# Kernel tuning notes

Measured on AMD Instinct MI355X. Metric: run time of the kernel, lower is better.

Reference implementation:

```python
import jax, jax.numpy as jnp
import numpy as np

N = 8192  # number of proposals


def setup_inputs() -> dict:
    key = jax.random.key(0)
    k1, k2, k3 = jax.random.split(key, 3)
    xy = jax.random.uniform(k1, (N, 2), dtype=jnp.float32) * 1000.0   # top-left corners
    wh = jax.random.uniform(k2, (N, 2), dtype=jnp.float32) * 120.0 + 4.0  # widths/heights
    conf = jax.random.uniform(k3, (N, 1), dtype=jnp.float32)
    preds = jnp.concatenate([xy, xy + wh, conf], axis=1)  # [N,5] x1,y1,x2,y2,conf
    return {"preds": preds, "thresh": 0.5, "max_proposals": 1000}


def _nms_keep_mask(boxes_sorted, thresh):
    # boxes_sorted: [N,4] sorted by descending confidence
    x1, y1, x2, y2 = (boxes_sorted[:, i] for i in range(4))
    area = (x2 - x1) * (y2 - y1)                               # [N]
    ix1 = jnp.maximum(x1[:, None], x1[None, :])
    iy1 = jnp.maximum(y1[:, None], y1[None, :])
    ix2 = jnp.minimum(x2[:, None], x2[None, :])
    iy2 = jnp.minimum(y2[:, None], y2[None, :])
    iw = jnp.maximum(ix2 - ix1, 0.0)
    ih = jnp.maximum(iy2 - iy1, 0.0)
    inter = iw * ih                                            # [N,N]
    iou = inter / (area[:, None] + area[None, :] - inter + 1e-12)
    n = boxes_sorted.shape[0]
    later = jnp.arange(n)[None, :] > jnp.arange(n)[:, None]    # strictly lower-priority boxes

    def body(i, keep):
        # if box i survives, suppress all later boxes overlapping it above thresh
        sup = keep[i] & later[i] & (iou[i] > thresh)
        return keep & ~sup

    return jax.lax.fori_loop(0, n, body, jnp.ones((n,), dtype=bool))


def reference(preds, thresh, max_proposals):
    # thresh < 0 -> identity (original early return); implemented with thresh >= 0 path
    order = jnp.argsort(-preds[:, 4])          # descending confidence
    boxes_sorted = preds[order, :4]
    keep = _nms_keep_mask(boxes_sorted, thresh)  # [N] bool, in sorted order
    n = preds.shape[0]
    # stable pack: kept positions first (ascending = descending confidence), pad at end
    rank = jnp.where(keep, jnp.arange(n), n)
    pos = jnp.argsort(rank)[:max_proposals]     # [M] positions in sorted order
    valid = keep[pos]                           # [M] which slots are real
    keep_idx = jnp.where(valid, order[pos], -1)  # indices into original preds, -1 pad
    kept = preds[jnp.clip(keep_idx, 0)]          # [M,5]
    kept = jnp.where(valid[:, None], kept, 0.0)
    return kept, keep_idx
```

## Files before the change

kernel.cpp:

```cpp
#include <hip/hip_runtime.h>

typedef unsigned long long u64;

#define FSLOTS 16
#define RCUT 2048

__device__ __forceinline__ u64 bcast64(u64 v, int b) {
  unsigned lo = __builtin_amdgcn_readlane((unsigned)v, b);
  unsigned hi = __builtin_amdgcn_readlane((unsigned)(v >> 32), b);
  return ((u64)hi << 32) | lo;
}
__device__ __forceinline__ u64 sgpr64(u64 v) {
  unsigned lo = __builtin_amdgcn_readfirstlane((unsigned)v);
  unsigned hi = __builtin_amdgcn_readfirstlane((unsigned)(v >> 32));
  return ((u64)hi << 32) | lo;
}
__device__ __forceinline__ u64 wor64(u64 v) {
#pragma unroll
  for (int off = 32; off; off >>= 1) v |= __shfl_xor(v, off, 64);
  return v;
}

#define APPLYJ(JV, T)                                                      \
  if ((T) < lim_) {                                                        \
    int j_ = (JV);                                                         \
    atomicAnd(&live[j_ >> 6], ~((u64)1 << (j_ & 63)));                     \
  }

#define CHUNK(c, BND, RC, LA, LB, LC, LD)                                  \
  if (out < maxp && (c) < nch) {                                           \
    u64 rem_ = sgpr64(live[(c)]);                                          \
    if (rem_) {                                                            \
      u64 K_;                                                              \
      u64 my_ = ((rem_ >> lane) & 1) ? (BND) : 0;                          \
      u64 A_ = sgpr64(wor64(my_));                                         \
      u64 hot_ = rem_ & A_;                                                \
      if (!hot_) {                                                         \
        K_ = rem_;                                                         \
      } else {                                                             \
        u64 defK_ = rem_ & ~A_;                                            \
        u64 myk_ = ((defK_ >> lane) & 1) ? (BND) : 0;                      \
        u64 S_ = sgpr64(wor64(myk_));                                      \
        K_ = defK_;                                                        \
        while (hot_) {                                                     \
          int b_ = __builtin_amdgcn_readfirstlane(                         \
              (int)__builtin_ctzll(hot_));                                 \
          hot_ &= hot_ - 1;                                                \
          if (!((S_ >> b_) & 1)) {                                         \
            K_ |= (u64)1 << b_;                                            \
            S_ |= bcast64(BND, b_);                                        \
          }                                                                \
        }                                                                  \
      }                                                                    \
      int kc_ = (int)__popcll(K_);                                         \
      bool mine_ = (K_ >> lane) & 1;                                       \
      if (mine_) {                                                         \
        int pos_ = out + (int)__popcll(K_ & (((u64)1 << lane) - 1));       \
        if (pos_ < maxp) sel[pos_] = (c) * 64 + lane;                      \
      }                                                                    \
      out += kc_;                                                          \
      if (kc_ > 0 && out < maxp) {                                         \
        int lim_ = mine_ ? ((RC) < FSLOTS ? (RC) : FSLOTS) : 0;            \
        APPLYJ((LA).x, 0)  APPLYJ((LA).y, 1)                               \
        APPLYJ((LA).z, 2)  APPLYJ((LA).w, 3)                               \
        APPLYJ((LB).x, 4)  APPLYJ((LB).y, 5)                               \
        APPLYJ((LB).z, 6)  APPLYJ((LB).w, 7)                               \
        APPLYJ((LC).x, 8)  APPLYJ((LC).y, 9)                               \
        APPLYJ((LC).z, 10) APPLYJ((LC).w, 11)                              \
        APPLYJ((LD).x, 12) APPLYJ((LD).y, 13)                              \
        APPLYJ((LD).z, 14) APPLYJ((LD).w, 15)                              \
        u64 ovf_ = __ballot(mine_ && (RC) > FSLOTS);                       \
        while (ovf_) {                                                     \
          int l_ = (int)__builtin_ctzll(ovf_);                             \
          ovf_ &= ovf_ - 1;                                                \
          int r_ = (c) * 64 + l_;                                          \
          u64 v0_ = (2 * lane < nch)                                       \
                        ? M[(size_t)r_ * nw + 2 * lane] : 0ULL;            \
          u64 v1_ = (2 * lane + 1 < nch)                                   \
                        ? M[(size_t)r_ * nw + 2 * lane + 1] : 0ULL;        \
          live[2 * lane] &= ~v0_;                                          \
          live[2 * lane + 1] &= ~v1_;                                      \
        }                                                                  \
      }                                                                    \
    }                                                                      \
    {                                                                      \
      int cc_ = (c) + 4;                                                   \
      if (cc_ < nch) {                                                     \
        int r_ = cc_ * 64 + lane;                                          \
        int rr_ = r_ < n ? r_ : n - 1;                                     \
        BND = D1[rr_];                                                     \
        RC = rowcnt[rr_];                                                  \
        const int4* lp_ = (const int4*)(rowlist + (size_t)rr_ * FSLOTS);   \
        LA = lp_[0]; LB = lp_[1]; LC = lp_[2]; LD = lp_[3];                \
      }                                                                    \
    }                                                                      \
  }

#define PREF(cc, BND, RC, LA, LB, LC, LD)                                  \
  if ((cc) < nch) {                                                        \
    int r_ = (cc) * 64 + lane;                                             \
    int rr_ = r_ < n ? r_ : n - 1;                                         \
    BND = D1[rr_];                                                         \
    RC = rowcnt[rr_];                                                      \
    const int4* lp_ = (const int4*)(rowlist + (size_t)rr_ * FSLOTS);       \
    LA = lp_[0]; LB = lp_[1]; LC = lp_[2]; LD = lp_[3];                    \
  }

#define SCAN_BODY(NCH_)                                                    \
  int nch = (NCH_);                                                        \
  for (int w = lane; w < 128; w += 64) {                                   \
    u64 m = 0;                                                             \
    if (w < nw) {                                                          \
      long long hi = (long long)(w + 1) * 64;                              \
      m = (hi <= n) ? ~0ULL                                                \
                    : ((n > (long long)w * 64)                             \
                           ? (((u64)1 << (n - w * 64)) - 1) : 0ULL);       \
    }                                                                      \
    live[w] = m;                                                           \
  }                                                                        \
  u64 b0 = 0, b1 = 0, b2 = 0, b3 = 0;                                      \
  int rc0 = 0, rc1 = 0, rc2 = 0, rc3 = 0;                                  \
  int4 l00 = {0,0,0,0}, l01 = {0,0,0,0}, l02 = {0,0,0,0}, l03 = {0,0,0,0}; \
  int4 l10 = {0,0,0,0}, l11 = {0,0,0,0}, l12 = {0,0,0,0}, l13 = {0,0,0,0}; \
  int4 l20 = {0,0,0,0}, l21 = {0,0,0,0}, l22 = {0,0,0,0}, l23 = {0,0,0,0}; \
  int4 l30 = {0,0,0,0}, l31 = {0,0,0,0}, l32 = {0,0,0,0}, l33 = {0,0,0,0}; \
  PREF(0, b0, rc0, l00, l01, l02, l03)                                     \
  PREF(1, b1, rc1, l10, l11, l12, l13)                                     \
  PREF(2, b2, rc2, l20, l21, l22, l23)                                     \
  PREF(3, b3, rc3, l30, l31, l32, l33)                                     \
  int out = 0;                                                             \
  for (int kk = 0; kk < nch && out < maxp; kk += 4) {                      \
    CHUNK(kk + 0, b0, rc0, l00, l01, l02, l03)                             \
    CHUNK(kk + 1, b1, rc1, l10, l11, l12, l13)                             \
    CHUNK(kk + 2, b2, rc2, l20, l21, l22, l23)                             \
    CHUNK(kk + 3, b3, rc3, l30, l31, l32, l33)                             \
  }

__device__ __forceinline__ void do_tile(int wx, int ry, int lane,
                                        const float4* sb4, float4* cb,
                                        float* cbar, int n, float th,
                                        u64* M, u64* D1, int* rowcnt,
                                        int* rowlist, int nw) {
  int col0 = wx * 64;
  int cj = col0 + lane;
  int cjc = cj < n ? cj : n - 1;
  {
    float4 b4 = sb4[cjc];
    cb[lane] = b4;
    cbar[lane] = __fmul_rn(__fsub_rn(b4.z, b4.x), __fsub_rn(b4.w, b4.y));
  }
  int row = ry * 64 + lane;
  if (row >= n) return;
  float4 r4 = sb4[row];
  float rarea = __fmul_rn(__fsub_rn(r4.z, r4.x), __fsub_rn(r4.w, r4.y));
  u64 w = 0;
#pragma unroll 8
  for (int j = 0; j < 64; ++j) {
    float4 c4 = cb[j];
    float ix1 = fmaxf(r4.x, c4.x);
    float iy1 = fmaxf(r4.y, c4.y);
    float ix2 = fminf(r4.z, c4.z);
    float iy2 = fminf(r4.w, c4.w);
    float iw = fmaxf(__fsub_rn(ix2, ix1), 0.0f);
    float ih = fmaxf(__fsub_rn(iy2, iy1), 0.0f);
    float inter = __fmul_rn(iw, ih);
    float denom = __fadd_rn(__fsub_rn(__fadd_rn(rarea, cbar[j]), inter), 1e-12f);
    float iou = __fdiv_rn(inter, denom);
    int col = col0 + j;
    bool sup = (col > row) && (col < n) && (iou > th);
    w |= ((u64)sup) << j;
  }
  M[(size_t)row * nw + wx] = w;
  if (wx == ry) D1[row] = w;
  int pcw = (int)__popcll(w);
  if (pcw) {
    int base = atomicAdd(&rowcnt[row], pcw);
    u64 w2 = w;
    int k = 0;
    while (w2) {
      int j = (int)__builtin_ctzll(w2);
      w2 &= w2 - 1;
      int idx = base + k;
      if (idx < FSLOTS) rowlist[(size_t)row * FSLOTS + idx] = col0 + j;
      ++k;
    }
  }
}

__device__ __forceinline__ void tri_decode(int u, int* wxo, int* ryo) {
  int w = (int)((sqrtf(8.0f * u + 1.0f) - 1.0f) * 0.5f);
  while ((w + 1) * (w + 2) / 2 <= u) ++w;
  while (w * (w + 1) / 2 > u) --w;
  *wxo = w;
  *ryo = u - w * (w + 1) / 2;
}

__global__ __launch_bounds__(256)
void k_rank(const float* __restrict__ preds, int n,
            float* __restrict__ sboxes, int* __restrict__ sidx,
            int* __restrict__ rowcnt) {
  __shared__ float cs[8192];
  int t = threadIdx.x;
  int b = blockIdx.x;
  for (int j = t; j < n; j += 256) cs[j] = preds[j * 5 + 4];
  {
    int zi = b * 32 + t;
    if (t < 32 && zi < n) rowcnt[zi] = 0;
  }
  __syncthreads();

  int row = b * 32 + (t >> 3);
  int sub = t & 7;
  int cw = (((n + 7) >> 3) + 3) & ~3;
  int cnt = 0;
  if (row < n) {
    float ci = cs[row];
    int start = sub * cw;
    int end = start + cw; if (end > n) end = n;
    const float4* cs4 = (const float4*)cs;
    int s4 = start >> 2, e4 = end >> 2;
    for (int j4 = s4; j4 < e4; ++j4) {
      float4 c4 = cs4[j4];
      int jb = j4 * 4;
      cnt += (c4.x > ci) || (c4.x == ci && (jb + 0) < row);
      cnt += (c4.y > ci) || (c4.y == ci && (jb + 1) < row);
      cnt += (c4.z > ci) || (c4.z == ci && (jb + 2) < row);
      cnt += (c4.w > ci) || (c4.w == ci && (jb + 3) < row);
    }
    for (int j = e4 * 4; j < end; ++j)
      cnt += (cs[j] > ci) || (cs[j] == ci && j < row);
  }
  cnt += __shfl_down(cnt, 4, 8);
  cnt += __shfl_down(cnt, 2, 8);
  cnt += __shfl_down(cnt, 1, 8);
  if (sub == 0 && row < n) {
    int pos = cnt;
    sboxes[pos * 4 + 0] = preds[row * 5 + 0];
    sboxes[pos * 4 + 1] = preds[row * 5 + 1];
    sboxes[pos * 4 + 2] = preds[row * 5 + 2];
    sboxes[pos * 4 + 3] = preds[row * 5 + 3];
    sidx[pos] = row;
  }
}

__global__ __launch_bounds__(64)
void k_mask_lo(const float* __restrict__ sboxes, int n,
               const float* __restrict__ thr_p,
               u64* __restrict__ M, u64* __restrict__ D1,
               int* __restrict__ rowcnt, int* __restrict__ rowlist, int nw) {
  __shared__ float4 cb[64];
  __shared__ float cbar[64];
  int wx, ry;
  tri_decode(blockIdx.x, &wx, &ry);
  do_tile(wx, ry, threadIdx.x, (const float4*)sboxes, cb, cbar, n, *thr_p,
          M, D1, rowcnt, rowlist, nw);
}

__global__ __launch_bounds__(64, 1)
void k_finish(u64* __restrict__ M, u64* __restrict__ D1,
              int* __restrict__ rowcnt, int* __restrict__ rowlist,
              const float* __restrict__ preds, const float* __restrict__ thr_p,
              const float* __restrict__ sboxes, const int* __restrict__ sidx,
              int n, int nw, int maxp, int Rw,
              float* __restrict__ outp) {
  __shared__ u64 live[128];
  __shared__ int selL[1024];
  __shared__ float4 cb[64];
  __shared__ float cbar[64];
  int lane = threadIdx.x;
  int* sel = selL;
  int nk;

  bool done;
  {
    SCAN_BODY(Rw)
    nk = (out < maxp) ? out : maxp;
    done = (out >= maxp || Rw >= nw);
  }

  if (!done) {
    int loTri = (Rw * (Rw + 1)) / 2;
    int totTri = (nw * (nw + 1)) / 2;
    float th = *thr_p;
    const float4* sb4 = (const float4*)sboxes;
    for (int u = loTri; u < totTri; ++u) {
      int wx, ry;
      tri_decode(u, &wx, &ry);
      do_tile(wx, ry, lane, sb4, cb, cbar, n, th,
              M, D1, rowcnt, rowlist, nw);
    }
    {
      SCAN_BODY(nw)
      nk = (out < maxp) ? out : maxp;
    }
  }

  for (int k = lane; k < maxp; k += 64) {
    if (k < nk) {
      int p = selL[k];
      int orig = sidx[p];
#pragma unroll
      for (int q = 0; q < 5; ++q) outp[k * 5 + q] = preds[orig * 5 + q];
      outp[(size_t)maxp * 5 + k] = (float)orig;
    } else {
#pragma unroll
      for (int q = 0; q < 5; ++q) outp[k * 5 + q] = 0.0f;
      outp[(size_t)maxp * 5 + k] = -1.0f;
    }
  }
}

extern "C" void kernel_launch(void* const* d_in, const int* in_sizes, int n_in,
                              void* d_out, int out_size, void* d_ws, size_t ws_size,
                              hipStream_t stream) {
  const float* preds = (const float*)d_in[0];
  const float* thr   = (const float*)d_in[1];
  float* out = (float*)d_out;
  int n    = in_sizes[0] / 5;
  int maxp = out_size / 6;
  int nw   = (n + 63) / 64;
  int Rw   = (RCUT / 64 < nw) ? RCUT / 64 : nw;
  int loTri = (Rw * (Rw + 1)) / 2;

  char* ws = (char*)d_ws;
  u64* M = (u64*)ws;
  size_t off = (size_t)n * nw * sizeof(u64);
  u64* D1 = (u64*)(ws + off);  off += (size_t)n * sizeof(u64);
  float* sboxes = (float*)(ws + off);  off += (size_t)n * 4 * sizeof(float);
  int*   sidx   = (int*)(ws + off);    off += (size_t)n * sizeof(int);
  int*   rowcnt = (int*)(ws + off);    off += (size_t)n * sizeof(int);
  int*   rowlist= (int*)(ws + off);

  hipLaunchKernelGGL(k_rank, dim3((n + 31) / 32), dim3(256), 0, stream,
                     preds, n, sboxes, sidx, rowcnt);
  hipLaunchKernelGGL(k_mask_lo, dim3(loTri), dim3(64), 0, stream,
                     sboxes, n, thr, M, D1, rowcnt, rowlist, nw);
  hipLaunchKernelGGL(k_finish, dim3(1), dim3(64), 0, stream,
                     M, D1, rowcnt, rowlist, preds, thr, sboxes, sidx,
                     n, nw, maxp, Rw, out);
}
```

Baseline: 70.29 us.

## Merge mask-tile and finish kernels into one launch with flag-based sync

The separate low-triangle mask kernel and single-block finish kernel become one launch. Block 0 spin-waits on per-tile release flags set by the other blocks before running the scan and greedy selection. This removes one kernel launch and the dependency gap between the two kernels. The cost is spin-polling on global flags, and correctness depends on all tile blocks being scheduled while block 0 waits. Block 0 could be resident first and occupy a slot, but with 528 small blocks that is likely fine.

After: 91.11 us. +29.6%, slower.

```diff
diff --git a/kernel.cpp b/kernel.cpp
--- a/kernel.cpp
+++ b/kernel.cpp
@@ -196,9 +196,9 @@
 }
 
 __global__ __launch_bounds__(256)
-void k_rank(const float* __restrict__ preds, int n,
+void k_prep(const float* __restrict__ preds, int n,
             float* __restrict__ sboxes, int* __restrict__ sidx,
-            int* __restrict__ rowcnt) {
+            int* __restrict__ rowcnt, int* __restrict__ flags) {
   __shared__ float cs[8192];
   int t = threadIdx.x;
   int b = blockIdx.x;
@@ -206,6 +206,9 @@
   {
     int zi = b * 32 + t;
     if (t < 32 && zi < n) rowcnt[zi] = 0;
+    if (b == 0) {
+      flags[t] = 0; flags[t + 256] = 0; flags[t + 512] = 0;
+    }
   }
   __syncthreads();
 
@@ -243,34 +246,41 @@
   }
 }
 
-__global__ __launch_bounds__(64)
-void k_mask_lo(const float* __restrict__ sboxes, int n,
-               const float* __restrict__ thr_p,
-               u64* __restrict__ M, u64* __restrict__ D1,
-               int* __restrict__ rowcnt, int* __restrict__ rowlist, int nw) {
-  __shared__ float4 cb[64];
-  __shared__ float cbar[64];
-  int wx, ry;
-  tri_decode(blockIdx.x, &wx, &ry);
-  do_tile(wx, ry, threadIdx.x, (const float4*)sboxes, cb, cbar, n, *thr_p,
-          M, D1, rowcnt, rowlist, nw);
-}
-
 __global__ __launch_bounds__(64, 1)
-void k_finish(u64* __restrict__ M, u64* __restrict__ D1,
-              int* __restrict__ rowcnt, int* __restrict__ rowlist,
-              const float* __restrict__ preds, const float* __restrict__ thr_p,
-              const float* __restrict__ sboxes, const int* __restrict__ sidx,
-              int n, int nw, int maxp, int Rw,
-              float* __restrict__ outp) {
+void k_main(u64* __restrict__ M, u64* __restrict__ D1,
+            int* __restrict__ rowcnt, int* __restrict__ rowlist,
+            const float* __restrict__ preds, const float* __restrict__ thr_p,
+            const float* __restrict__ sboxes, const int* __restrict__ sidx,
+            int n, int nw, int maxp, int Rw, int loTri,
+            int* __restrict__ flags, float* __restrict__ outp) {
   __shared__ u64 live[128];
   __shared__ int selL[1024];
   __shared__ float4 cb[64];
   __shared__ float cbar[64];
   int lane = threadIdx.x;
+  int bid = blockIdx.x;
+  const float4* sb4 = (const float4*)sboxes;
+
+  if (bid != 0) {
+    float th = *thr_p;
+    int wx, ry;
+    tri_decode(bid - 1, &wx, &ry);
+    do_tile(wx, ry, lane, sb4, cb, cbar, n, th, M, D1, rowcnt, rowlist, nw);
+    if (lane == 0) {
+      __threadfence();
+      __hip_atomic_store(&flags[bid], 1, __ATOMIC_RELEASE,
+                         __HIP_MEMORY_SCOPE_AGENT);
+    }
+    return;
+  }
+
+  for (int f = 1 + lane; f <= loTri; f += 64)
+    while (__hip_atomic_load(&flags[f], __ATOMIC_ACQUIRE,
+                             __HIP_MEMORY_SCOPE_AGENT) == 0) {}
+  __builtin_amdgcn_wave_barrier();
+
   int* sel = selL;
   int nk;
-
   bool done;
   {
     SCAN_BODY(Rw)
@@ -279,15 +289,12 @@
   }
 
   if (!done) {
-    int loTri = (Rw * (Rw + 1)) / 2;
     int totTri = (nw * (nw + 1)) / 2;
     float th = *thr_p;
-    const float4* sb4 = (const float4*)sboxes;
     for (int u = loTri; u < totTri; ++u) {
       int wx, ry;
       tri_decode(u, &wx, &ry);
-      do_tile(wx, ry, lane, sb4, cb, cbar, n, th,
-              M, D1, rowcnt, rowlist, nw);
+      do_tile(wx, ry, lane, sb4, cb, cbar, n, th, M, D1, rowcnt, rowlist, nw);
     }
     {
       SCAN_BODY(nw)
@@ -329,13 +336,12 @@
   float* sboxes = (float*)(ws + off);  off += (size_t)n * 4 * sizeof(float);
   int*   sidx   = (int*)(ws + off);    off += (size_t)n * sizeof(int);
   int*   rowcnt = (int*)(ws + off);    off += (size_t)n * sizeof(int);
-  int*   rowlist= (int*)(ws + off);
-
-  hipLaunchKernelGGL(k_rank, dim3((n + 31) / 32), dim3(256), 0, stream,
-                     preds, n, sboxes, sidx, rowcnt);
-  hipLaunchKernelGGL(k_mask_lo, dim3(loTri), dim3(64), 0, stream,
-                     sboxes, n, thr, M, D1, rowcnt, rowlist, nw);
-  hipLaunchKernelGGL(k_finish, dim3(1), dim3(64), 0, stream,
+  int*   rowlist= (int*)(ws + off);    off += (size_t)n * FSLOTS * sizeof(int);
+  int*   flags  = (int*)(ws + off);
+
+  hipLaunchKernelGGL(k_prep, dim3((n + 31) / 32), dim3(256), 0, stream,
+                     preds, n, sboxes, sidx, rowcnt, flags);
+  hipLaunchKernelGGL(k_main, dim3(loTri + 1), dim3(64), 0, stream,
                      M, D1, rowcnt, rowlist, preds, thr, sboxes, sidx,
-                     n, nw, maxp, Rw, out);
-}
+                     n, nw, maxp, Rw, loTri, flags, out);
+}
```
